# Optimization experiments

Hardware: AMD Instinct MI355X
Metric: run time of the kernel (lower is better)

Reference implementation:

```python
import jax, jax.numpy as jnp
import numpy as np

N = 50000   # num_entities
F = 300     # node feature dim
D = 128     # embedding_dim
H = 4       # heads
C = D // H  # per-head out channels (32)
E = 640000  # num edges
R = 200     # num_relations
L = 2       # num_layers
NEG_SLOPE = 0.2  # PyG GATv2Conv default


def setup_inputs() -> dict:
    key = jax.random.key(0)
    ks = jax.random.split(key, 14)
    s = 0.1
    return {
        "entity": jnp.arange(N, dtype=jnp.int32),
        "edge_index": jax.random.randint(ks[0], (2, E), 0, N, dtype=jnp.int32),
        "edge_type": jax.random.randint(ks[1], (E,), 0, R, dtype=jnp.int32),
        # learned parameters
        "node_features": jax.random.normal(ks[2], (N, F), jnp.float32) * s,   # entity_embedding table
        "rel_emb": jax.random.normal(ks[3], (R, D), jnp.float32) * s,          # relation_embedding
        "proj_w": jax.random.normal(ks[4], (F, D), jnp.float32) * s,           # project Linear
        "proj_b": jnp.zeros((D,), jnp.float32),
        # per-layer GATv2Conv params, stacked over L layers
        "w_l": jax.random.normal(ks[5], (L, D, H * C), jnp.float32) * s,       # lin_l weight
        "b_l": jnp.zeros((L, H * C), jnp.float32),
        "w_r": jax.random.normal(ks[6], (L, D, H * C), jnp.float32) * s,       # lin_r weight
        "b_r": jnp.zeros((L, H * C), jnp.float32),
        "w_e": jax.random.normal(ks[7], (L, D, H * C), jnp.float32) * s,       # lin_edge weight (no bias)
        "att": jax.random.normal(ks[8], (L, H, C), jnp.float32) * s,           # attention vector a
        "bias": jnp.zeros((L, H * C), jnp.float32),                             # output bias
    }


def _gatv2_layer(x, src, dst, edge_attr, w_l, b_l, w_r, b_r, w_e, att, bias):
    # x: [N, D], edge_attr: [E, D]
    x_l = (x @ w_l + b_l).reshape(N, H, C)
    x_r = (x @ w_r + b_r).reshape(N, H, C)
    e = (edge_attr @ w_e).reshape(E, H, C)
    # per-edge message (gather src/dst + edge), GATv2: leaky_relu BEFORE attention dot
    m = jax.nn.leaky_relu(x_l[src] + x_r[dst] + e, NEG_SLOPE)   # [E, H, C]
    logits = jnp.einsum('ehc,hc->eh', m, att)                    # [E, H]
    # segment softmax over edges grouped by destination node
    lmax = jax.ops.segment_max(logits, dst, num_segments=N)      # [N, H]
    ex = jnp.exp(logits - lmax[dst])                             # [E, H]
    denom = jax.ops.segment_sum(ex, dst, num_segments=N)         # [N, H]
    alpha = ex / denom[dst]                                      # [E, H]
    # scatter-aggregate messages x_l[src] weighted by alpha
    out = jax.ops.segment_sum(x_l[src] * alpha[:, :, None], dst, num_segments=N)  # [N, H, C]
    return out.reshape(N, H * C) + bias


def reference(entity, edge_index, edge_type, node_features, rel_emb,
              proj_w, proj_b, w_l, b_l, w_r, b_r, w_e, att, bias):
    x = node_features[entity]            # embedding lookup
    x = x @ proj_w + proj_b              # project to D
    edge_attr = rel_emb[edge_type]       # [E, D] (weights=False -> no edge_weight scaling)
    src, dst = edge_index[0], edge_index[1]
    for i in range(L):
        x = _gatv2_layer(x, src, dst, edge_attr,
                         w_l[i], b_l[i], w_r[i], b_r[i], w_e[i], att[i], bias[i])
        if i != L - 1:
            x = jax.nn.elu(x)            # dropout inactive (eval mode)
    return x
```

## Files before the change

kernel.cpp:

```cpp
#include <hip/hip_runtime.h>

#define NN 50000
#define FF 300
#define DD 128
#define HH 4
#define CC 32
#define EE 640000
#define RR 200
#define LL 2
#define SB ((NN + 255) / 256)
#define PK 320
#define WCONV (2 * 128 * 128)
#define WTOT (2 * 128 * PK + WCONV)
#define HB ((EE + 255) / 256)
#define WB (WCONV / 256)
#define FB PK
#define RB (LL * RR / 2)

typedef unsigned short u16;
typedef unsigned int u32;
typedef _Float16 h2   __attribute__((ext_vector_type(2)));
typedef _Float16 half8 __attribute__((ext_vector_type(8)));
typedef __attribute__((ext_vector_type(4))) float floatx4;
typedef u32 u32x4 __attribute__((ext_vector_type(4)));

__device__ __forceinline__ u16 f2h(float f) {
    union { _Float16 h; u16 u; } v; v.h = (_Float16)f; return v.u;
}
__device__ __forceinline__ float h2f(u16 u) {
    union { u16 u; _Float16 h; } v; v.u = u; return (float)v.h;
}
__device__ __forceinline__ h2 u2h2(u32 p) {
    union { u32 u; h2 h; } v; v.u = p; return v.h;
}
__device__ __forceinline__ h2 hmax2(h2 a, h2 b) {
#if __has_builtin(__builtin_elementwise_max)
    return __builtin_elementwise_max(a, b);
#else
    h2 r; r.x = a.x > b.x ? a.x : b.x; r.y = a.y > b.y ? a.y : b.y; return r;
#endif
}
__device__ __forceinline__ float hdot2(h2 a, h2 b, float c) {
#if __has_builtin(__builtin_amdgcn_fdot2)
    return __builtin_amdgcn_fdot2(a, b, c, false);
#else
    return c + (float)a.x * (float)b.x + (float)a.y * (float)b.y;
#endif
}

__device__ __forceinline__ int block_excl_scan(int v, int* lds4, int* total) {
    int lane = threadIdx.x & 63, wid = threadIdx.x >> 6;
    int x = v;
    #pragma unroll
    for (int off = 1; off < 64; off <<= 1) {
        int y = __shfl_up(x, off, 64);
        if (lane >= off) x += y;
    }
    if (lane == 63) lds4[wid] = x;
    __syncthreads();
    int add = 0;
    #pragma unroll
    for (int w = 0; w < 4; w++) add += (w < wid) ? lds4[w] : 0;
    *total = lds4[0] + lds4[1] + lds4[2] + lds4[3];
    return x + add - v;
}

__global__ __launch_bounds__(256)
void prep_kernel(const int* __restrict__ ei, int* __restrict__ counts,
                 const float* __restrict__ proj_w, const float* __restrict__ w_l,
                 const float* __restrict__ w_r, u16* __restrict__ wt,
                 const float* __restrict__ rel_emb, const float* __restrict__ w_e,
                 u16* __restrict__ erel, const float* __restrict__ proj_b,
                 const float* __restrict__ b_l, const float* __restrict__ b_r,
                 float* __restrict__ fbias)
{
    __shared__ float rv[2][DD];
    int b = blockIdx.x, tid = threadIdx.x;
    if (b < HB) {
        int e = b * 256 + tid;
        if (e < EE) atomicAdd(&counts[ei[EE + e]], 1);
    } else if (b < HB + WB) {
        int i = (b - HB) * 256 + tid;
        int seg = i >> 14;
        int r = i & 16383;
        int n = r >> 7, k = r & 127;
        const float* src = (seg == 0 ? w_l : w_r) + (size_t)DD * DD;
        wt[2 * 128 * PK + i] = f2h(src[(size_t)k * DD + n]);
    } else if (b < HB + WB + FB) {
        int half = tid >> 7, d = tid & 127;
        int pp = (b - HB - WB) * 2 + half;
        int lr = pp / PK, k = pp - lr * PK;
        rv[half][d] = (k < FF) ? proj_w[(size_t)k * DD + d] : 0.f;
        __syncthreads();
        float acc = 0.f;
        if (k < FF) {
            const float* W = lr ? w_r : w_l;
            #pragma unroll 8
            for (int j = 0; j < DD; j++) acc += rv[half][j] * W[(size_t)j * DD + d];
        }
        wt[(size_t)lr * 128 * PK + (size_t)d * PK + k] = f2h(acc);
    } else if (b == HB + WB + FB) {
        int half = tid >> 7, d = tid & 127;
        if (tid < DD) rv[0][tid] = proj_b[tid];
        __syncthreads();
        const float* W = half ? w_r : w_l;
        float acc = half ? b_r[d] : b_l[d];
        #pragma unroll 8
        for (int j = 0; j < DD; j++) acc += rv[0][j] * W[(size_t)j * DD + d];
        fbias[half * DD + d] = acc;
    } else {
        int half = tid >> 7, d = tid & 127;
        int lr = (b - HB - WB - FB - 1) * 2 + half;
        int l = lr / RR, r = lr - l * RR;
        rv[half][d] = rel_emb[r * DD + d];
        __syncthreads();
        const float* W = w_e + (size_t)l * DD * DD;
        float acc = 0.f;
        #pragma unroll 8
        for (int k = 0; k < DD; k++) acc += rv[half][k] * W[k * DD + d];
        erel[(size_t)lr * DD + d] = f2h(acc);
    }
}

template<bool AF16, bool GATHER, int K>
__global__ __launch_bounds__(512)
void gemm8_kernel(const void* __restrict__ A_, const int* __restrict__ rowidx,
                  int lda, int Ka,
                  const u16* __restrict__ BT1, const float* __restrict__ bias1,
                  u16* __restrict__ C1,
                  const u16* __restrict__ BT2, const float* __restrict__ bias2,
                  u16* __restrict__ C2, int M)
{
    __shared__ u16 As[64][K + 8];
    int tid  = threadIdx.x;
    int m0   = blockIdx.x * 64;
    int wave = tid >> 6, lane = tid & 63;
    int quad = lane >> 4, l16 = lane & 15;
    const u16* BT = (wave < 4) ? BT1 : BT2;
    int wcol = (wave & 3) * 32;

    floatx4 acc[4][2];
    #pragma unroll
    for (int i = 0; i < 4; i++)
        #pragma unroll
        for (int j = 0; j < 2; j++) acc[i][j] = (floatx4){0.f, 0.f, 0.f, 0.f};

    const u16* Brow[2];
    #pragma unroll
    for (int j = 0; j < 2; j++) Brow[j] = BT + (size_t)(wcol + j * 16 + l16) * K;

    half8 bfc[2];
    #pragma unroll
    for (int j = 0; j < 2; j++) bfc[j] = *(const half8*)(Brow[j] + quad * 8);

    int ar = tid >> 3, at = tid & 7;
    int arow = m0 + ar;
    int rid = (arow < M) ? (GATHER ? rowidx[arow] : arow) : 0;
    #pragma unroll
    for (int c = 0; c < K / 64; c++) {
        int kb = c * 64 + at * 8;
        u16 tmp[8];
        if (AF16) {
            const u16* Ap = (const u16*)A_ + (size_t)rid * lda + kb;
            *(half8*)tmp = *(const half8*)Ap;
        } else {
            const float* Ap = (const float*)A_ + (size_t)rid * lda + kb;
            if (kb + 8 <= Ka) {
                float4 f0 = *(const float4*)Ap;
                float4 f1 = *(const float4*)(Ap + 4);
                tmp[0] = f2h(f0.x); tmp[1] = f2h(f0.y); tmp[2] = f2h(f0.z); tmp[3] = f2h(f0.w);
                tmp[4] = f2h(f1.x); tmp[5] = f2h(f1.y); tmp[6] = f2h(f1.z); tmp[7] = f2h(f1.w);
            } else {
                #pragma unroll
                for (int jj = 0; jj < 8; jj++) tmp[jj] = (kb + jj < Ka) ? f2h(Ap[jj]) : (u16)0;
            }
        }
        *(half8*)&As[ar][kb] = *(half8*)tmp;
    }
    __syncthreads();

    #pragma unroll
    for (int kk = 0; kk < K; kk += 32) {
        half8 bfn[2];
        if (kk + 32 < K) {
            #pragma unroll
            for (int j = 0; j < 2; j++)
                bfn[j] = *(const half8*)(Brow[j] + kk + 32 + quad * 8);
        }
        half8 af[4];
        #pragma unroll
        for (int i = 0; i < 4; i++)
            af[i] = *(const half8*)&As[i * 16 + l16][kk + quad * 8];
        #pragma unroll
        for (int i = 0; i < 4; i++)
            #pragma unroll
            for (int j = 0; j < 2; j++)
                acc[i][j] = __builtin_amdgcn_mfma_f32_16x16x32_f16(
                    af[i], bfc[j], acc[i][j], 0, 0, 0);
        bfc[0] = bfn[0]; bfc[1] = bfn[1];
    }

    u16* Cw = (wave < 4) ? C1 : C2;
    const float* bw = (wave < 4) ? bias1 : bias2;
    #pragma unroll
    for (int i = 0; i < 4; i++) {
        #pragma unroll
        for (int rr = 0; rr < 4; rr++) {
            int row = m0 + i * 16 + quad * 4 + rr;
            if (row < M) {
                #pragma unroll
                for (int j = 0; j < 2; j++) {
                    int col = wcol + j * 16 + l16;
                    Cw[(size_t)row * DD + col] = f2h(acc[i][j][rr] + bw[col]);
                }
            }
        }
    }
}

__global__ __launch_bounds__(256)
void scan_local_kernel(const int* __restrict__ counts, int* __restrict__ offsets,
                       int* __restrict__ bsum)
{
    __shared__ int lds4[4];
    int i = blockIdx.x * 256 + threadIdx.x;
    int v = (i < NN) ? counts[i] : 0;
    int total;
    int ex = block_excl_scan(v, lds4, &total);
    if (i < NN) offsets[i] = ex;
    if (threadIdx.x == 0) bsum[blockIdx.x] = total;
}

__global__ __launch_bounds__(256)
void scan_bsum_kernel(int* __restrict__ bsum)
{
    __shared__ int lds4[4];
    int t = threadIdx.x;
    int v = (t < SB) ? bsum[t] : 0;
    int total;
    int ex = block_excl_scan(v, lds4, &total);
    if (t < SB) bsum[t] = ex;
}

__global__ __launch_bounds__(256)
void scatter_kernel(const int* __restrict__ ei, const int* __restrict__ et,
                    const int* __restrict__ offsets, const int* __restrict__ bsum,
                    int* __restrict__ fill, u32* __restrict__ dstorder)
{
    int e = blockIdx.x * 256 + threadIdx.x;
    if (e >= EE) return;
    int d = ei[EE + e];
    int pos = offsets[d] + bsum[d >> 8] + atomicAdd(&fill[d], 1);
    dstorder[pos] = (u32)ei[e] | ((u32)et[e] << 16);
}

__global__ __launch_bounds__(256)
void node_kernel(const u32* __restrict__ dstorder, const int* __restrict__ offsets,
                 const int* __restrict__ bsum,
                 const u16* __restrict__ xl, const u16* __restrict__ xr,
                 const u16* __restrict__ erel, const float* __restrict__ att,
                 const float* __restrict__ bias,
                 u16* __restrict__ xnext, float* __restrict__ outp, int is_last)
{
    int tid  = threadIdx.x;
    int node = blockIdx.x * 4 + (tid >> 6);
    int lane = tid & 63;
    if (node >= NN) return;
    int g  = lane >> 4;
    int gl = lane & 15;
    int c0 = gl * 8;
    int beg = offsets[node] + bsum[node >> 8];
    int end = (node == NN - 1) ? EE : offsets[node + 1] + bsum[(node + 1) >> 8];

    h2 xrh[4], atth[4];
    {
        u32x4 xrv = *(const u32x4*)(xr + ((u32)node * DD + c0));
        #pragma unroll
        for (int q = 0; q < 4; q++) xrh[q] = u2h2(xrv[q]);
        #pragma unroll
        for (int q = 0; q < 4; q++) {
            float2 av = *(const float2*)&att[c0 + q * 2];
            atth[q] = (h2){(_Float16)av.x, (_Float16)av.y};
        }
    }
    const h2 c02 = (h2){(_Float16)0.2f, (_Float16)0.2f};

    float s = 0.f;
    h2 a2[4];
    #pragma unroll
    for (int q = 0; q < 4; q++) a2[q] = (h2){(_Float16)0.f, (_Float16)0.f};

    for (int base = beg; base < end; base += 4) {
        int es = base + g;
        bool valid = es < end;
        u32 st = valid ? dstorder[es] : 0;
        u32 xoff = (st & 0xffffu) * DD + (u32)c0;
        u32 eoff = (st >> 16) * DD + (u32)c0;
        u32x4 xv = *(const u32x4*)(xl + xoff);
        u32x4 ev = *(const u32x4*)(erel + eoff);
        h2 xh[4];
        float p = 0.f;
        #pragma unroll
        for (int q = 0; q < 4; q++) {
            xh[q] = u2h2(xv[q]);
            h2 m = (xh[q] + xrh[q]) + u2h2(ev[q]);
            m = hmax2(m, m * c02);
            p = hdot2(m, atth[q], p);
        }
        p += __shfl_xor(p, 1, 64);
        p += __shfl_xor(p, 2, 64);
        float w = valid ? __expf(fminf(p, 60.f)) : 0.f;
        s += w;
        h2 wh = (h2){(_Float16)w, (_Float16)w};
        #pragma unroll
        for (int q = 0; q < 4; q++) a2[q] += wh * xh[q];
    }

    float a[8];
    #pragma unroll
    for (int q = 0; q < 4; q++) { a[q*2] = (float)a2[q].x; a[q*2+1] = (float)a2[q].y; }
    #pragma unroll
    for (int j = 0; j < 8; j++) {
        a[j] += __shfl_xor(a[j], 16, 64);
        a[j] += __shfl_xor(a[j], 32, 64);
    }
    s += __shfl_xor(s, 16, 64);
    s += __shfl_xor(s, 32, 64);

    if (lane < 16) {
        float rh = 1.f / fmaxf(s, 1e-30f);
        float4 b0 = *(const float4*)&bias[c0];
        float4 b1 = *(const float4*)&bias[c0 + 4];
        float bv[8] = {b0.x, b0.y, b0.z, b0.w, b1.x, b1.y, b1.z, b1.w};
        float v[8];
        #pragma unroll
        for (int j = 0; j < 8; j++) v[j] = a[j] * rh + bv[j];
        if (is_last) {
            float4* op = (float4*)(outp + ((u32)node * DD + c0));
            op[0] = make_float4(v[0], v[1], v[2], v[3]);
            op[1] = make_float4(v[4], v[5], v[6], v[7]);
        } else {
            u16 pk[8];
            #pragma unroll
            for (int j = 0; j < 8; j++) {
                float w2 = v[j] > 0.f ? v[j] : __expf(v[j]) - 1.f;
                pk[j] = f2h(w2);
            }
            *(half8*)(xnext + ((u32)node * DD + c0)) = *(half8*)pk;
        }
    }
}

extern "C" void kernel_launch(void* const* d_in, const int* in_sizes, int n_in,
                              void* d_out, int out_size, void* d_ws, size_t ws_size,
                              hipStream_t stream)
{
    const int*   entity        = (const int*)d_in[0];
    const int*   edge_index    = (const int*)d_in[1];
    const int*   edge_type     = (const int*)d_in[2];
    const float* node_features = (const float*)d_in[3];
    const float* rel_emb       = (const float*)d_in[4];
    const float* proj_w        = (const float*)d_in[5];
    const float* proj_b        = (const float*)d_in[6];
    const float* w_l           = (const float*)d_in[7];
    const float* b_l           = (const float*)d_in[8];
    const float* w_r           = (const float*)d_in[9];
    const float* b_r           = (const float*)d_in[10];
    const float* w_e           = (const float*)d_in[11];
    const float* att           = (const float*)d_in[12];
    const float* bias          = (const float*)d_in[13];

    u16*   xb      = (u16*)d_ws;
    u16*   xl      = xb + (size_t)NN * DD;
    u16*   xr      = xl + (size_t)NN * DD;
    u16*   erel    = xr + (size_t)NN * DD;
    u16*   wt      = erel + (size_t)LL * RR * DD;
    u32*   dstorder= (u32*)(wt + WTOT);
    int*   counts  = (int*)(dstorder + (size_t)EE);
    int*   fill    = counts + NN;
    int*   offsets = fill + NN;
    int*   bsum    = offsets + NN;
    float* fbias   = (float*)(bsum + SB);

    hipMemsetAsync(counts, 0, (size_t)NN * 2 * sizeof(int), stream);
    prep_kernel<<<HB + WB + FB + 1 + RB, 256, 0, stream>>>(
        edge_index, counts, proj_w, w_l, w_r, wt, rel_emb, w_e, erel,
        proj_b, b_l, b_r, fbias);

    scan_local_kernel<<<SB, 256, 0, stream>>>(counts, offsets, bsum);
    scan_bsum_kernel<<<1, 256, 0, stream>>>(bsum);
    scatter_kernel<<<(EE + 255) / 256, 256, 0, stream>>>(
        edge_index, edge_type, offsets, bsum, fill, dstorder);

    const int GB2 = (NN + 63) / 64;

    gemm8_kernel<false, true, PK><<<GB2, 512, 0, stream>>>(
        node_features, entity, FF, FF,
        wt, fbias, xl,
        wt + (size_t)128 * PK, fbias + DD, xr, NN);
    node_kernel<<<(NN + 3) / 4, 256, 0, stream>>>(
        dstorder, offsets, bsum, xl, xr, erel,
        att, bias, xb, (float*)d_out, 0);

    gemm8_kernel<true, false, DD><<<GB2, 512, 0, stream>>>(
        xb, nullptr, DD, DD,
        wt + (size_t)2 * 128 * PK, b_l + DD, xl,
        wt + (size_t)2 * 128 * PK + 128 * 128, b_r + DD, xr, NN);
    node_kernel<<<(NN + 3) / 4, 256, 0, stream>>>(
        dstorder, offsets, bsum, xl, xr, erel + (size_t)RR * DD,
        att + DD, bias + DD, xb, (float*)d_out, 1);
}
```

Measured before the change: 325.0 us.

## Pre-convert node features to fp16 and stage GEMM tiles via global_load_lds

Adds a conversion pass in the prep kernel that gathers node features by entity into a padded fp16 buffer. Both node GEMMs are replaced with a kernel that copies A and B tiles straight from global memory into XOR-swizzled LDS using global_load_lds, looping over K in 64-wide chunks. The aim is to cut per-block fp32 conversion work and register-staged loads, and to share B tiles through LDS. In exchange it adds an extra write and read of a 50000x320 fp16 buffer, and the new main loop has two barriers per K step with no double buffering.

Measured after the change: 318.5 us. 2.0% less time.

```diff
diff --git a/kernel.cpp b/kernel.cpp
--- a/kernel.cpp
+++ b/kernel.cpp
@@ -16,9 +16,11 @@
 #define WB (WCONV / 256)
 #define FB PK
 #define RB (LL * RR / 2)
+#define CVB ((NN * (PK / 8) + 255) / 256)
 
 typedef unsigned short u16;
 typedef unsigned int u32;
+typedef unsigned long long u64;
 typedef _Float16 h2   __attribute__((ext_vector_type(2)));
 typedef _Float16 half8 __attribute__((ext_vector_type(8)));
 typedef __attribute__((ext_vector_type(4))) float floatx4;
@@ -26,9 +28,6 @@
 
 __device__ __forceinline__ u16 f2h(float f) {
     union { _Float16 h; u16 u; } v; v.h = (_Float16)f; return v.u;
-}
-__device__ __forceinline__ float h2f(u16 u) {
-    union { u16 u; _Float16 h; } v; v.u = u; return (float)v.h;
 }
 __device__ __forceinline__ h2 u2h2(u32 p) {
     union { u32 u; h2 h; } v; v.u = p; return v.h;
@@ -46,6 +45,11 @@
 #else
     return c + (float)a.x * (float)b.x + (float)a.y * (float)b.y;
 #endif
+}
+__device__ __forceinline__ void glds16(const void* g, void* l) {
+    using gp = const unsigned int __attribute__((address_space(1)))*;
+    using lp = unsigned int __attribute__((address_space(3)))*;
+    __builtin_amdgcn_global_load_lds((gp)(u64)g, (lp)(u64)l, 16, 0, 0);
 }
 
 __device__ __forceinline__ int block_excl_scan(int v, int* lds4, int* total) {
@@ -72,7 +76,8 @@
                  const float* __restrict__ rel_emb, const float* __restrict__ w_e,
                  u16* __restrict__ erel, const float* __restrict__ proj_b,
                  const float* __restrict__ b_l, const float* __restrict__ b_r,
-                 float* __restrict__ fbias)
+                 float* __restrict__ fbias, const int* __restrict__ entity,
+                 const float* __restrict__ nf, u16* __restrict__ xh)
 {
     __shared__ float rv[2][DD];
     int b = blockIdx.x, tid = threadIdx.x;
@@ -108,7 +113,7 @@
         #pragma unroll 8
         for (int j = 0; j < DD; j++) acc += rv[0][j] * W[(size_t)j * DD + d];
         fbias[half * DD + d] = acc;
-    } else {
+    } else if (b < HB + WB + FB + 1 + RB) {
         int half = tid >> 7, d = tid & 127;
         int lr = (b - HB - WB - FB - 1) * 2 + half;
         int l = lr / RR, r = lr - l * RR;
@@ -119,25 +124,42 @@
         #pragma unroll 8
         for (int k = 0; k < DD; k++) acc += rv[half][k] * W[k * DD + d];
         erel[(size_t)lr * DD + d] = f2h(acc);
-    }
-}
-
-template<bool AF16, bool GATHER, int K>
+    } else {
+        int ci = (b - (HB + WB + FB + 1 + RB)) * 256 + tid;
+        if (ci < NN * (PK / 8)) {
+            int row = ci / (PK / 8);
+            int col = (ci - row * (PK / 8)) * 8;
+            int xrow = entity[row];
+            const float* src = nf + (size_t)xrow * FF + col;
+            u16 o[8];
+            if (col + 8 <= FF) {
+                float4 f0 = *(const float4*)src;
+                float4 f1 = *(const float4*)(src + 4);
+                o[0] = f2h(f0.x); o[1] = f2h(f0.y); o[2] = f2h(f0.z); o[3] = f2h(f0.w);
+                o[4] = f2h(f1.x); o[5] = f2h(f1.y); o[6] = f2h(f1.z); o[7] = f2h(f1.w);
+            } else {
+                #pragma unroll
+                for (int j = 0; j < 8; j++) o[j] = (col + j < FF) ? f2h(src[j]) : (u16)0;
+            }
+            *(half8*)(xh + (size_t)row * PK + col) = *(half8*)o;
+        }
+    }
+}
+
+template<int K>
 __global__ __launch_bounds__(512)
-void gemm8_kernel(const void* __restrict__ A_, const int* __restrict__ rowidx,
-                  int lda, int Ka,
-                  const u16* __restrict__ BT1, const float* __restrict__ bias1,
-                  u16* __restrict__ C1,
-                  const u16* __restrict__ BT2, const float* __restrict__ bias2,
-                  u16* __restrict__ C2, int M)
-{
-    __shared__ u16 As[64][K + 8];
+void gemm_gll_kernel(const u16* __restrict__ A,
+                     const u16* __restrict__ BT1, const float* __restrict__ bias1,
+                     u16* __restrict__ C1,
+                     const u16* __restrict__ BT2, const float* __restrict__ bias2,
+                     u16* __restrict__ C2, int M)
+{
+    __shared__ u16 As[64 * 64];
+    __shared__ u16 Bs[256 * 64];
     int tid  = threadIdx.x;
     int m0   = blockIdx.x * 64;
     int wave = tid >> 6, lane = tid & 63;
     int quad = lane >> 4, l16 = lane & 15;
-    const u16* BT = (wave < 4) ? BT1 : BT2;
-    int wcol = (wave & 3) * 32;
 
     floatx4 acc[4][2];
     #pragma unroll
@@ -145,63 +167,53 @@
         #pragma unroll
         for (int j = 0; j < 2; j++) acc[i][j] = (floatx4){0.f, 0.f, 0.f, 0.f};
 
-    const u16* Brow[2];
-    #pragma unroll
-    for (int j = 0; j < 2; j++) Brow[j] = BT + (size_t)(wcol + j * 16 + l16) * K;
-
-    half8 bfc[2];
-    #pragma unroll
-    for (int j = 0; j < 2; j++) bfc[j] = *(const half8*)(Brow[j] + quad * 8);
-
-    int ar = tid >> 3, at = tid & 7;
-    int arow = m0 + ar;
-    int rid = (arow < M) ? (GATHER ? rowidx[arow] : arow) : 0;
-    #pragma unroll
-    for (int c = 0; c < K / 64; c++) {
-        int kb = c * 64 + at * 8;
-        u16 tmp[8];
-        if (AF16) {
-            const u16* Ap = (const u16*)A_ + (size_t)rid * lda + kb;
-            *(half8*)tmp = *(const half8*)Ap;
-        } else {
-            const float* Ap = (const float*)A_ + (size_t)rid * lda + kb;
-            if (kb + 8 <= Ka) {
-                float4 f0 = *(const float4*)Ap;
-                float4 f1 = *(const float4*)(Ap + 4);
-                tmp[0] = f2h(f0.x); tmp[1] = f2h(f0.y); tmp[2] = f2h(f0.z); tmp[3] = f2h(f0.w);
-                tmp[4] = f2h(f1.x); tmp[5] = f2h(f1.y); tmp[6] = f2h(f1.z); tmp[7] = f2h(f1.w);
-            } else {
-                #pragma unroll
-                for (int jj = 0; jj < 8; jj++) tmp[jj] = (kb + jj < Ka) ? f2h(Ap[jj]) : (u16)0;
-            }
-        }
-        *(half8*)&As[ar][kb] = *(half8*)tmp;
-    }
-    __syncthreads();
-
-    #pragma unroll
-    for (int kk = 0; kk < K; kk += 32) {
-        half8 bfn[2];
-        if (kk + 32 < K) {
+    int arl = wave * 8 + (lane >> 3);
+    int arg = m0 + arl; if (arg >= M) arg = M - 1;
+    const char* ap = (const char*)(A + (size_t)arg * K)
+                   + (((lane & 7) << 4) ^ ((arl & 7) << 4));
+    const char* bp[4];
+    #pragma unroll
+    for (int c = 0; c < 4; c++) {
+        int rowB = wave * 32 + c * 8 + (lane >> 3);
+        const u16* base = (rowB < 128) ? BT1 : BT2;
+        int br = rowB & 127;
+        bp[c] = (const char*)(base + (size_t)br * K)
+              + (((lane & 7) << 4) ^ ((br & 7) << 4));
+    }
+    char* AsW = (char*)As;
+    char* BsW = (char*)Bs;
+    const char* AsR = (const char*)As;
+    const char* BsR = (const char*)Bs;
+    int axor = (l16 & 7) << 4;
+
+    for (int kk = 0; kk < K; kk += 64) {
+        glds16(ap + kk * 2, AsW + wave * 1024);
+        #pragma unroll
+        for (int c = 0; c < 4; c++)
+            glds16(bp[c] + kk * 2, BsW + (wave * 4 + c) * 1024);
+        __syncthreads();
+        #pragma unroll
+        for (int s2 = 0; s2 < 2; s2++) {
+            int cb = (s2 * 64 + quad * 16) ^ axor;
+            half8 af[4], bf[2];
+            #pragma unroll
+            for (int i = 0; i < 4; i++)
+                af[i] = *(const half8*)(AsR + (i * 16 + l16) * 128 + cb);
             #pragma unroll
             for (int j = 0; j < 2; j++)
-                bfn[j] = *(const half8*)(Brow[j] + kk + 32 + quad * 8);
-        }
-        half8 af[4];
-        #pragma unroll
-        for (int i = 0; i < 4; i++)
-            af[i] = *(const half8*)&As[i * 16 + l16][kk + quad * 8];
-        #pragma unroll
-        for (int i = 0; i < 4; i++)
+                bf[j] = *(const half8*)(BsR + (wave * 32 + j * 16 + l16) * 128 + cb);
             #pragma unroll
-            for (int j = 0; j < 2; j++)
-                acc[i][j] = __builtin_amdgcn_mfma_f32_16x16x32_f16(
-                    af[i], bfc[j], acc[i][j], 0, 0, 0);
-        bfc[0] = bfn[0]; bfc[1] = bfn[1];
+            for (int i = 0; i < 4; i++) {
+                acc[i][0] = __builtin_amdgcn_mfma_f32_16x16x32_f16(af[i], bf[0], acc[i][0], 0, 0, 0);
+                acc[i][1] = __builtin_amdgcn_mfma_f32_16x16x32_f16(af[i], bf[1], acc[i][1], 0, 0, 0);
+            }
+        }
+        __syncthreads();
     }
 
     u16* Cw = (wave < 4) ? C1 : C2;
     const float* bw = (wave < 4) ? bias1 : bias2;
+    int cb0 = (wave & 3) * 32;
     #pragma unroll
     for (int i = 0; i < 4; i++) {
         #pragma unroll
@@ -210,7 +222,7 @@
             if (row < M) {
                 #pragma unroll
                 for (int j = 0; j < 2; j++) {
-                    int col = wcol + j * 16 + l16;
+                    int col = cb0 + j * 16 + l16;
                     Cw[(size_t)row * DD + col] = f2h(acc[i][j][rr] + bw[col]);
                 }
             }
@@ -381,11 +393,12 @@
     int*   offsets = fill + NN;
     int*   bsum    = offsets + NN;
     float* fbias   = (float*)(bsum + SB);
+    u16*   xh      = (u16*)(fbias + 2 * DD);
 
     hipMemsetAsync(counts, 0, (size_t)NN * 2 * sizeof(int), stream);
-    prep_kernel<<<HB + WB + FB + 1 + RB, 256, 0, stream>>>(
+    prep_kernel<<<HB + WB + FB + 1 + RB + CVB, 256, 0, stream>>>(
         edge_index, counts, proj_w, w_l, w_r, wt, rel_emb, w_e, erel,
-        proj_b, b_l, b_r, fbias);
+        proj_b, b_l, b_r, fbias, entity, node_features, xh);
 
     scan_local_kernel<<<SB, 256, 0, stream>>>(counts, offsets, bsum);
     scan_bsum_kernel<<<1, 256, 0, stream>>>(bsum);
@@ -394,17 +407,15 @@
 
     const int GB2 = (NN + 63) / 64;
 
-    gemm8_kernel<false, true, PK><<<GB2, 512, 0, stream>>>(
-        node_features, entity, FF, FF,
-        wt, fbias, xl,
+    gemm_gll_kernel<PK><<<GB2, 512, 0, stream>>>(
+        xh, wt, fbias, xl,
         wt + (size_t)128 * PK, fbias + DD, xr, NN);
     node_kernel<<<(NN + 3) / 4, 256, 0, stream>>>(
         dstorder, offsets, bsum, xl, xr, erel,
         att, bias, xb, (float*)d_out, 0);
 
-    gemm8_kernel<true, false, DD><<<GB2, 512, 0, stream>>>(
-        xb, nullptr, DD, DD,
-        wt + (size_t)2 * 128 * PK, b_l + DD, xl,
+    gemm_gll_kernel<DD><<<GB2, 512, 0, stream>>>(
+        xb, wt + (size_t)2 * 128 * PK, b_l + DD, xl,
         wt + (size_t)2 * 128 * PK + 128 * 128, b_r + DD, xr, NN);
     node_kernel<<<(NN + 3) / 4, 256, 0, stream>>>(
         dstorder, offsets, bsum, xl, xr, erel + (size_t)RR * DD,
```
